# Optimization experiments

Measured on AMD Instinct MI355X. Metric: run time of the kernel, lower is better.

The kernel has to match this reference:

```python
import jax, jax.numpy as jnp
import numpy as np

D = 128  # input_depth == output_depth
NUM_NODES_PATTERN = np.tile(np.array([32, 48, 64, 96], dtype=np.int64), 64)  # G=256 graphs


def _build_indices(nn_np):
    """Per pair-entry (row-major within each n_g x n_g block): global row node,
    global col node, graph id, diagonal mask; plus per-node graph id / size."""
    G = len(nn_np)
    offs = np.zeros(G, dtype=np.int64)
    offs[1:] = np.cumsum(nn_np)[:-1]
    rows_l, cols_l, g_l, diag_l = [], [], [], []
    for gi, (n, o) in enumerate(zip(nn_np, offs)):
        i = np.repeat(np.arange(n, dtype=np.int64), n)  # row index within block
        j = np.tile(np.arange(n, dtype=np.int64), n)    # col index within block
        rows_l.append(o + i)
        cols_l.append(o + j)
        g_l.append(np.full(n * n, gi, dtype=np.int64))
        diag_l.append(i == j)
    rows = np.concatenate(rows_l)
    cols = np.concatenate(cols_l)
    g_edge = np.concatenate(g_l)
    diag = np.concatenate(diag_l)
    g_node = np.repeat(np.arange(G, dtype=np.int64), nn_np)  # graph of each node
    n_node = np.repeat(nn_np, nn_np)                          # n_g of each node
    N = int(nn_np.sum())
    return rows, cols, g_edge, diag, g_node, n_node, N, G


def setup_inputs() -> dict:
    key = jax.random.key(0)
    nn_np = NUM_NODES_PATTERN
    E = int(np.sum(nn_np ** 2))  # 1,064,960 pair entries
    N = int(nn_np.sum())         # 15,360 nodes
    k1, k2, k3 = jax.random.split(key, 3)
    x = jax.random.normal(k1, (E, D), dtype=jnp.float32)
    coeffs = jax.random.normal(k2, (D, D, 5), dtype=jnp.float32) * float(np.sqrt(2.0) / (D + D))
    bias = jnp.zeros((1, D), dtype=jnp.float32)
    edges_index = jax.random.randint(k3, (2, E), 0, N, dtype=jnp.int64)  # unused by the layer
    num_nodes = jnp.asarray(nn_np)
    return {"x": x, "coeffs": coeffs, "bias": bias,
            "edges_index": edges_index, "num_nodes": num_nodes}


def reference(x, coeffs, bias, edges_index, num_nodes):
    # edges_index is unused, matching the original forward.
    nn_np = np.asarray(num_nodes)
    rows, cols, g_edge, diag, g_node, n_node, N, G = _build_indices(nn_np)
    seg = jax.ops.segment_sum
    diag_m = jnp.asarray(diag)[:, None].astype(x.dtype)  # [E,1]
    n = jnp.asarray(n_node).astype(x.dtype)[:, None]     # [N,1] block size per node

    op1 = seg(x * diag_m, jnp.asarray(rows), num_segments=N)          # diag part (unnormalized)
    op3 = seg(x, jnp.asarray(rows), num_segments=N) / n               # row sums / n
    op4 = seg(x, jnp.asarray(cols), num_segments=N) / n               # col sums / n
    diag_g = seg(x * diag_m, jnp.asarray(g_edge), num_segments=G)     # [G,d] trace per graph
    all_g = seg(x, jnp.asarray(g_edge), num_segments=G)               # [G,d] total sum per graph
    gn = jnp.asarray(g_node)
    op2 = diag_g[gn] / n                                              # trace broadcast / n
    op5 = all_g[gn] / (n * n)                                         # total broadcast / n^2

    ops = jnp.stack([op1, op2, op3, op4, op5], axis=2)                # [N, d, 5]
    out = jnp.einsum('dsb,ndb->ns', coeffs, ops) + bias               # [N, output_depth]
    return out
```

## Files before the change

### kernel.cpp

```cpp
#include <hip/hip_runtime.h>

#define D 128


template<int CTRL>
__device__ __forceinline__ float f_dpp_add(float v) {
    return v + __int_as_float(__builtin_amdgcn_update_dpp(
        0, __float_as_int(v), CTRL, 0xF, 0xF, true));
}

#define DPP_ROR8 0x128

__device__ __forceinline__ float f_xor16_sum(float v) {
#if __has_builtin(__builtin_amdgcn_permlane16_swap)
    typedef int v2i __attribute__((ext_vector_type(2)));
    v2i r = __builtin_amdgcn_permlane16_swap(__float_as_int(v), __float_as_int(v),
                                             false, false);
    return __int_as_float(r[0]) + __int_as_float(r[1]);
#else
    return v + __shfl_xor(v, 16);
#endif
}

__device__ __forceinline__ float f_xor32_sum(float v) {
#if __has_builtin(__builtin_amdgcn_permlane32_swap)
    typedef int v2i __attribute__((ext_vector_type(2)));
    v2i r = __builtin_amdgcn_permlane32_swap(__float_as_int(v), __float_as_int(v),
                                             false, false);
    return __int_as_float(r[0]) + __int_as_float(r[1]);
#else
    return v + __shfl_xor(v, 32);
#endif
}

__device__ __forceinline__ void f4add(float4& a, const float4& b) {
    a.x += b.x; a.y += b.y; a.z += b.z; a.w += b.w;
}

__device__ __forceinline__ void f4_jreduce_full(float4& a) {
    a.x = f_dpp_add<DPP_ROR8>(a.x);
    a.y = f_dpp_add<DPP_ROR8>(a.y);
    a.z = f_dpp_add<DPP_ROR8>(a.z);
    a.w = f_dpp_add<DPP_ROR8>(a.w);
    a.x = f_xor16_sum(a.x);
    a.y = f_xor16_sum(a.y);
    a.z = f_xor16_sum(a.z);
    a.w = f_xor16_sum(a.w);
    a.x = f_xor32_sum(a.x);
    a.y = f_xor32_sum(a.y);
    a.z = f_xor32_sum(a.z);
    a.w = f_xor32_sum(a.w);
}

template<int N>
__device__ __forceinline__ void run_class(const float* __restrict__ x,
                                          long ebase, int o, int gidx, int chunk,
                                          float* __restrict__ diagG,
                                          float* __restrict__ rowG,
                                          float* __restrict__ colG,
                                          float* __restrict__ trG,
                                          float* __restrict__ totG,
                                          float4* __restrict__ rowtile ,
                                          float4* __restrict__ red     ) {
    constexpr int NW = (N < 64 ? N / 8 : 8);
    const int tid = threadIdx.x;
    const int l   = tid & 63;
    const int w   = tid >> 6;
    const int f4  = l & 7;
    const int j0  = tid >> 3;
    constexpr bool TWO = (N > 64);
    const bool act0 = (j0 < N);
    const bool act1 = TWO && (w < 4);
    const float invn = 1.0f / (float)N;

    const float4* x4 = reinterpret_cast<const float4*>(x);
    const long istride = (long)N * 32;
    const long e0 = (ebase + j0) * 32 + chunk * 8 + f4;

    float4 c0 = {0,0,0,0}, c1 = {0,0,0,0};

    int buf = 0;
    for (int t0 = 0; t0 < N; t0 += 16, buf ^= 1) {
        if (act0) {
            const float4* p0 = x4 + e0 + (long)t0 * istride;
            const float4* p1 = p0 + 64L * 32;
            float4* wt = rowtile + ((buf * 16) * 8 + w) * 8 + f4;
#pragma unroll 4
            for (int r = 0; r < 16; ++r) {
                float4 v = p0[(long)r * istride];
                f4add(c0, v);
                if (TWO && act1) {
                    float4 u = p1[(long)r * istride];
                    f4add(c1, u);
                    f4add(v, u);
                }
                f4_jreduce_full(v);
                if (l < 8) wt[r * 64] = v;
            }
        }
        __syncthreads();
        {
            const int rr = tid >> 5;
            const int dd = tid & 31;
            const float* rp = reinterpret_cast<const float*>(rowtile)
                            + (buf * 16 + rr) * 256 + dd;
            float acc = 0.f;
#pragma unroll
            for (int w2 = 0; w2 < NW; ++w2) acc += rp[w2 * 32];
            rowG[(long)(o + t0 + rr) * D + chunk * 32 + dd] = acc * invn;
        }
    }

    float4 d0 = {0,0,0,0}, d1 = {0,0,0,0};
    if (act0) d0 = x4[e0 + (long)j0 * istride];
    if (TWO && act1) d1 = x4[e0 + 64L * 32 + (long)(j0 + 64) * istride];

    float4* diag4 = reinterpret_cast<float4*>(diagG);
    float4* col4  = reinterpret_cast<float4*>(colG);
    if (act0) {
        diag4[(long)(o + j0) * 32 + chunk * 8 + f4] = d0;
        col4 [(long)(o + j0) * 32 + chunk * 8 + f4] = c0;
    }
    if (TWO && act1) {
        diag4[(long)(o + j0 + 64) * 32 + chunk * 8 + f4] = d1;
        col4 [(long)(o + j0 + 64) * 32 + chunk * 8 + f4] = c1;
    }

    {
        float4 td = d0; if (TWO) f4add(td, d1);
        float4 tc = c0; if (TWO) f4add(tc, c1);
        f4_jreduce_full(td);
        f4_jreduce_full(tc);
        if (l < 8) {
            red[w * 8 + f4]      = td;
            red[64 + w * 8 + f4] = tc;
        }
    }
    __syncthreads();
    float4* tr4  = reinterpret_cast<float4*>(trG);
    float4* tot4 = reinterpret_cast<float4*>(totG);
    if (tid < 8) {
        float4 a = {0,0,0,0};
#pragma unroll
        for (int w2 = 0; w2 < NW; ++w2) f4add(a, red[w2 * 8 + tid]);
        tr4[gidx * 32 + chunk * 8 + tid] = a;
    } else if (tid < 16) {
        const int f = tid - 8;
        float4 a = {0,0,0,0};
#pragma unroll
        for (int w2 = 0; w2 < NW; ++w2) f4add(a, red[64 + w2 * 8 + f]);
        tot4[gidx * 32 + chunk * 8 + f] = a;
    }
}

__global__ __launch_bounds__(512) void k1_reduce(const float* __restrict__ x,
                                                 float* __restrict__ diagG,
                                                 float* __restrict__ rowG,
                                                 float* __restrict__ colG,
                                                 float* __restrict__ trG,
                                                 float* __restrict__ totG) {
    __shared__ float4 rowtile[2048];
    __shared__ float4 red[128];

    const int b  = blockIdx.x;
    const int bb = b & 255;
    const int k  = bb >> 2;
    const int chunk = bb & 3;

    if (b < 256) {
        run_class<96>(x, 16640L * k + 7424, 240 * k + 144, 4 * k + 3, chunk, diagG, rowG, colG, trG, totG, rowtile, red);
    } else if (b < 512) {
        run_class<64>(x, 16640L * k + 3328, 240 * k + 80, 4 * k + 2, chunk, diagG, rowG, colG, trG, totG, rowtile, red);
    } else if (b < 768) {
        run_class<48>(x, 16640L * k + 1024, 240 * k + 32, 4 * k + 1, chunk, diagG, rowG, colG, trG, totG, rowtile, red);
    } else {
        run_class<32>(x, 16640L * k, 240 * k, 4 * k, chunk, diagG, rowG, colG, trG, totG, rowtile, red);
    }
}

__global__ void k0_transpose(const float* __restrict__ coeffs, float* __restrict__ Wt) {
    int d = blockIdx.x;
    int s = threadIdx.x;
    const float* cp = coeffs + ((long)d * D + s) * 5;
#pragma unroll
    for (int b = 0; b < 5; ++b) Wt[b * (D * D) + d * D + s] = cp[b];
}

__global__ __launch_bounds__(128) void k2_pg(const float* __restrict__ trG,
                                             const float* __restrict__ totG,
                                             const float* __restrict__ Wt,
                                             const float* __restrict__ bias,
                                             float* __restrict__ pg) {
    __shared__ float tr[D], tt[D];
    const int ns_[4] = {32, 48, 64, 96};
    int g = blockIdx.x;
    int c = g & 3;
    float invn = 1.0f / (float)ns_[c];

    int s = threadIdx.x;
    tr[s] = trG[g * D + s] * invn;
    tt[s] = totG[g * D + s] * invn * invn;
    __syncthreads();

    const float* W1 = Wt + 1 * D * D;
    const float* W4 = Wt + 4 * D * D;
    float acc = 0.f;
#pragma unroll 4
    for (int dd = 0; dd < D; ++dd)
        acc += W1[dd * D + s] * tr[dd] + W4[dd * D + s] * tt[dd];
    pg[g * D + s] = bias[s] + acc;
}

__global__ __launch_bounds__(512) void k3_gemm(const float* __restrict__ diagG,
                                               const float* __restrict__ rowG,
                                               const float* __restrict__ colG,
                                               const float* __restrict__ Wt,
                                               const float* __restrict__ pg,
                                               float* __restrict__ out) {
    __shared__ __align__(16) float ash[3][64][D];
    __shared__ int gish[64];
    const int nd0 = blockIdx.x * 64;
    const int tid = threadIdx.x;

    const float4* diag4 = reinterpret_cast<const float4*>(diagG);
    const float4* row4  = reinterpret_cast<const float4*>(rowG);
    const float4* col4  = reinterpret_cast<const float4*>(colG);

    for (int idx = tid; idx < 64 * 32; idx += 512) {
        int nn = idx >> 5;
        int q  = idx & 31;
        int nd = nd0 + nn;
        int p  = nd / 240;
        int r  = nd - p * 240;
        int c, n;
        if (r < 32)       { c = 0; n = 32; }
        else if (r < 80)  { c = 1; n = 48; }
        else if (r < 144) { c = 2; n = 64; }
        else              { c = 3; n = 96; }
        float invn = 1.0f / (float)n;
        float4 dv = diag4[(long)nd * 32 + q];
        float4 rv = row4[(long)nd * 32 + q];
        float4 cv = col4[(long)nd * 32 + q];
        cv.x *= invn; cv.y *= invn; cv.z *= invn; cv.w *= invn;
        *reinterpret_cast<float4*>(&ash[0][nn][q * 4]) = dv;
        *reinterpret_cast<float4*>(&ash[1][nn][q * 4]) = rv;
        *reinterpret_cast<float4*>(&ash[2][nn][q * 4]) = cv;
        if (q == 0) gish[nn] = 4 * p + c;
    }
    __syncthreads();

    const int s4 = tid & 31;
    const int nq = tid >> 5;
    const float* W0 = Wt;
    const float* W2 = Wt + 2 * D * D;
    const float* W3 = Wt + 3 * D * D;

    float4 acc[4];
#pragma unroll
    for (int a = 0; a < 4; ++a) acc[a] = make_float4(0.f, 0.f, 0.f, 0.f);

    for (int d4 = 0; d4 < 32; ++d4) {
        float4 w0[4], w2[4], w3[4];
#pragma unroll
        for (int dd = 0; dd < 4; ++dd) {
            const int d = d4 * 4 + dd;
            w0[dd] = *reinterpret_cast<const float4*>(&W0[d * D + s4 * 4]);
            w2[dd] = *reinterpret_cast<const float4*>(&W2[d * D + s4 * 4]);
            w3[dd] = *reinterpret_cast<const float4*>(&W3[d * D + s4 * 4]);
        }
#pragma unroll
        for (int a = 0; a < 4; ++a) {
            const int nn = nq * 4 + a;
            float4 a0 = *reinterpret_cast<const float4*>(&ash[0][nn][d4 * 4]);
            float4 a1 = *reinterpret_cast<const float4*>(&ash[1][nn][d4 * 4]);
            float4 a2 = *reinterpret_cast<const float4*>(&ash[2][nn][d4 * 4]);
            const float* a0f = reinterpret_cast<const float*>(&a0);
            const float* a1f = reinterpret_cast<const float*>(&a1);
            const float* a2f = reinterpret_cast<const float*>(&a2);
#pragma unroll
            for (int dd = 0; dd < 4; ++dd) {
                acc[a].x += w0[dd].x * a0f[dd] + w2[dd].x * a1f[dd] + w3[dd].x * a2f[dd];
                acc[a].y += w0[dd].y * a0f[dd] + w2[dd].y * a1f[dd] + w3[dd].y * a2f[dd];
                acc[a].z += w0[dd].z * a0f[dd] + w2[dd].z * a1f[dd] + w3[dd].z * a2f[dd];
                acc[a].w += w0[dd].w * a0f[dd] + w2[dd].w * a1f[dd] + w3[dd].w * a2f[dd];
            }
        }
    }

#pragma unroll
    for (int a = 0; a < 4; ++a) {
        const int nn = nq * 4 + a;
        const int nd = nd0 + nn;
        const int g  = gish[nn];
        float4 pgv = *reinterpret_cast<const float4*>(&pg[g * D + s4 * 4]);
        float4 r_;
        r_.x = acc[a].x + pgv.x;
        r_.y = acc[a].y + pgv.y;
        r_.z = acc[a].z + pgv.z;
        r_.w = acc[a].w + pgv.w;
        *reinterpret_cast<float4*>(&out[(long)nd * D + s4 * 4]) = r_;
    }
}

extern "C" void kernel_launch(void* const* d_in, const int* in_sizes, int n_in,
                              void* d_out, int out_size, void* d_ws, size_t ws_size,
                              hipStream_t stream) {
    const float* x      = (const float*)d_in[0];
    const float* coeffs = (const float*)d_in[1];
    const float* bias   = (const float*)d_in[2];

    float* ws    = (float*)d_ws;
    float* Wt    = ws;
    float* diagG = Wt + 81920;
    float* rowG  = diagG + 1966080;
    float* colG  = rowG + 1966080;
    float* pg    = colG + 1966080;
    float* trG   = pg + 32768;
    float* totG  = trG + 32768;
    float* out   = (float*)d_out;

    k0_transpose<<<128, 128, 0, stream>>>(coeffs, Wt);
    k1_reduce<<<1024, 512, 0, stream>>>(x, diagG, rowG, colG, trG, totG);
    k2_pg<<<256, 128, 0, stream>>>(trG, totG, Wt, bias, pg);
    k3_gemm<<<240, 512, 0, stream>>>(diagG, rowG, colG, Wt, pg, out);
}
```

Measured before the change: 202.7 us.

## Split reduction into per-class kernels over row blocks with atomic column/graph sums

Replaces the single reduction kernel, where each block walked a whole graph block for one feature chunk, with four templated kernels (one per graph size) whose blocks each handle only 16 rows. Column sums and per-graph trace and total sums are now built with float atomic adds into zeroed buffers, which needs an added memset. The goal is much more block-level parallelism and occupancy for streaming x, at the cost of many atomics, extra launches and a non-deterministic summation order.

```diff
diff --git a/kernel.cpp b/kernel.cpp
--- a/kernel.cpp
+++ b/kernel.cpp
@@ -52,129 +52,96 @@
     a.w = f_xor32_sum(a.w);
 }
 
-template<int N>
-__device__ __forceinline__ void run_class(const float* __restrict__ x,
-                                          long ebase, int o, int gidx, int chunk,
-                                          float* __restrict__ diagG,
-                                          float* __restrict__ rowG,
-                                          float* __restrict__ colG,
-                                          float* __restrict__ trG,
-                                          float* __restrict__ totG,
-                                          float4* __restrict__ rowtile ,
-                                          float4* __restrict__ red     ) {
-    constexpr int NW = (N < 64 ? N / 8 : 8);
+template<int N, int WPE>
+__global__ __launch_bounds__(N * 8, WPE)
+void k1_class(const float* __restrict__ x,
+              float* __restrict__ diagG, float* __restrict__ rowG,
+              float* __restrict__ colG, float* __restrict__ trG,
+              float* __restrict__ totG,
+              int EP, int NP, int CI) {
+    constexpr int NW  = N / 8;
+    constexpr int NRB = N / 16;
+    __shared__ __align__(16) float4 rowtile[16 * NW * 8];
+    __shared__ __align__(16) float4 red[2 * NW * 8];
+
     const int tid = threadIdx.x;
     const int l   = tid & 63;
     const int w   = tid >> 6;
     const int f4  = l & 7;
     const int j0  = tid >> 3;
-    constexpr bool TWO = (N > 64);
-    const bool act0 = (j0 < N);
-    const bool act1 = TWO && (w < 4);
+
+    const int b  = blockIdx.x;
+    const int rb = b % NRB;
+    const int ch = (b / NRB) & 3;
+    const int k  = b / (NRB * 4);
+    const long ebase = 16640L * k + EP;
+    const int  o     = 240 * k + NP;
+    const int  gi    = 4 * k + CI;
+    const int  r0    = rb * 16;
     const float invn = 1.0f / (float)N;
 
     const float4* x4 = reinterpret_cast<const float4*>(x);
     const long istride = (long)N * 32;
-    const long e0 = (ebase + j0) * 32 + chunk * 8 + f4;
-
-    float4 c0 = {0,0,0,0}, c1 = {0,0,0,0};
-
-    int buf = 0;
-    for (int t0 = 0; t0 < N; t0 += 16, buf ^= 1) {
-        if (act0) {
-            const float4* p0 = x4 + e0 + (long)t0 * istride;
-            const float4* p1 = p0 + 64L * 32;
-            float4* wt = rowtile + ((buf * 16) * 8 + w) * 8 + f4;
+    const long e0 = (ebase + (long)r0 * N + j0) * 32 + ch * 8 + f4;
+
+    float4 c0 = {0,0,0,0};
 #pragma unroll 4
-            for (int r = 0; r < 16; ++r) {
-                float4 v = p0[(long)r * istride];
-                f4add(c0, v);
-                if (TWO && act1) {
-                    float4 u = p1[(long)r * istride];
-                    f4add(c1, u);
-                    f4add(v, u);
-                }
-                f4_jreduce_full(v);
-                if (l < 8) wt[r * 64] = v;
-            }
-        }
-        __syncthreads();
-        {
-            const int rr = tid >> 5;
-            const int dd = tid & 31;
-            const float* rp = reinterpret_cast<const float*>(rowtile)
-                            + (buf * 16 + rr) * 256 + dd;
-            float acc = 0.f;
-#pragma unroll
-            for (int w2 = 0; w2 < NW; ++w2) acc += rp[w2 * 32];
-            rowG[(long)(o + t0 + rr) * D + chunk * 32 + dd] = acc * invn;
-        }
-    }
-
-    float4 d0 = {0,0,0,0}, d1 = {0,0,0,0};
-    if (act0) d0 = x4[e0 + (long)j0 * istride];
-    if (TWO && act1) d1 = x4[e0 + 64L * 32 + (long)(j0 + 64) * istride];
-
-    float4* diag4 = reinterpret_cast<float4*>(diagG);
-    float4* col4  = reinterpret_cast<float4*>(colG);
-    if (act0) {
-        diag4[(long)(o + j0) * 32 + chunk * 8 + f4] = d0;
-        col4 [(long)(o + j0) * 32 + chunk * 8 + f4] = c0;
-    }
-    if (TWO && act1) {
-        diag4[(long)(o + j0 + 64) * 32 + chunk * 8 + f4] = d1;
-        col4 [(long)(o + j0 + 64) * 32 + chunk * 8 + f4] = c1;
+    for (int r = 0; r < 16; ++r) {
+        float4 v = x4[e0 + (long)r * istride];
+        f4add(c0, v);
+        f4_jreduce_full(v);
+        if (l < 8) rowtile[(r * NW + w) * 8 + f4] = v;
+    }
+    __syncthreads();
+
+    for (int idx = tid; idx < 512; idx += N * 8) {
+        const int rr = idx >> 5;
+        const int dd = idx & 31;
+        const float* rp = reinterpret_cast<const float*>(rowtile) + rr * NW * 32 + dd;
+        float acc = 0.f;
+#pragma unroll
+        for (int w2 = 0; w2 < NW; ++w2) acc += rp[w2 * 32];
+        rowG[(long)(o + r0 + rr) * D + ch * 32 + dd] = acc * invn;
     }
 
     {
-        float4 td = d0; if (TWO) f4add(td, d1);
-        float4 tc = c0; if (TWO) f4add(tc, c1);
-        f4_jreduce_full(td);
-        f4_jreduce_full(tc);
-        if (l < 8) {
-            red[w * 8 + f4]      = td;
-            red[64 + w * 8 + f4] = tc;
-        }
+        float* cg = &colG[(long)(o + j0) * D + ch * 32 + f4 * 4];
+        unsafeAtomicAdd(cg + 0, c0.x);
+        unsafeAtomicAdd(cg + 1, c0.y);
+        unsafeAtomicAdd(cg + 2, c0.z);
+        unsafeAtomicAdd(cg + 3, c0.w);
+    }
+
+    float4 d0 = {0,0,0,0};
+    const bool hasdiag = (j0 >= r0) && (j0 < r0 + 16);
+    if (hasdiag) {
+        d0 = x4[(ebase + (long)j0 * N + j0) * 32 + ch * 8 + f4];
+        reinterpret_cast<float4*>(diagG)[(long)(o + j0) * 32 + ch * 8 + f4] = d0;
+    }
+
+    float4 td = d0, tc = c0;
+    f4_jreduce_full(td);
+    f4_jreduce_full(tc);
+    if (l < 8) {
+        red[w * 8 + f4]          = td;
+        red[NW * 8 + w * 8 + f4] = tc;
     }
     __syncthreads();
-    float4* tr4  = reinterpret_cast<float4*>(trG);
-    float4* tot4 = reinterpret_cast<float4*>(totG);
     if (tid < 8) {
         float4 a = {0,0,0,0};
 #pragma unroll
         for (int w2 = 0; w2 < NW; ++w2) f4add(a, red[w2 * 8 + tid]);
-        tr4[gidx * 32 + chunk * 8 + tid] = a;
+        float* tg = &trG[gi * D + ch * 32 + tid * 4];
+        unsafeAtomicAdd(tg + 0, a.x); unsafeAtomicAdd(tg + 1, a.y);
+        unsafeAtomicAdd(tg + 2, a.z); unsafeAtomicAdd(tg + 3, a.w);
     } else if (tid < 16) {
         const int f = tid - 8;
         float4 a = {0,0,0,0};
 #pragma unroll
-        for (int w2 = 0; w2 < NW; ++w2) f4add(a, red[64 + w2 * 8 + f]);
-        tot4[gidx * 32 + chunk * 8 + f] = a;
-    }
-}
-
-__global__ __launch_bounds__(512) void k1_reduce(const float* __restrict__ x,
-                                                 float* __restrict__ diagG,
-                                                 float* __restrict__ rowG,
-                                                 float* __restrict__ colG,
-                                                 float* __restrict__ trG,
-                                                 float* __restrict__ totG) {
-    __shared__ float4 rowtile[2048];
-    __shared__ float4 red[128];
-
-    const int b  = blockIdx.x;
-    const int bb = b & 255;
-    const int k  = bb >> 2;
-    const int chunk = bb & 3;
-
-    if (b < 256) {
-        run_class<96>(x, 16640L * k + 7424, 240 * k + 144, 4 * k + 3, chunk, diagG, rowG, colG, trG, totG, rowtile, red);
-    } else if (b < 512) {
-        run_class<64>(x, 16640L * k + 3328, 240 * k + 80, 4 * k + 2, chunk, diagG, rowG, colG, trG, totG, rowtile, red);
-    } else if (b < 768) {
-        run_class<48>(x, 16640L * k + 1024, 240 * k + 32, 4 * k + 1, chunk, diagG, rowG, colG, trG, totG, rowtile, red);
-    } else {
-        run_class<32>(x, 16640L * k, 240 * k, 4 * k, chunk, diagG, rowG, colG, trG, totG, rowtile, red);
+        for (int w2 = 0; w2 < NW; ++w2) f4add(a, red[NW * 8 + w2 * 8 + f]);
+        float* tg = &totG[gi * D + ch * 32 + f * 4];
+        unsafeAtomicAdd(tg + 0, a.x); unsafeAtomicAdd(tg + 1, a.y);
+        unsafeAtomicAdd(tg + 2, a.z); unsafeAtomicAdd(tg + 3, a.w);
     }
 }
 
@@ -314,13 +281,20 @@
     float* diagG = Wt + 81920;
     float* rowG  = diagG + 1966080;
     float* colG  = rowG + 1966080;
-    float* pg    = colG + 1966080;
-    float* trG   = pg + 32768;
+    float* trG   = colG + 1966080;
     float* totG  = trG + 32768;
+    float* pg    = totG + 32768;
     float* out   = (float*)d_out;
 
+    hipMemsetAsync(colG, 0, (1966080 + 32768 + 32768) * sizeof(float), stream);
+
     k0_transpose<<<128, 128, 0, stream>>>(coeffs, Wt);
-    k1_reduce<<<1024, 512, 0, stream>>>(x, diagG, rowG, colG, trG, totG);
+
+    k1_class<96, 6><<<1536, 768, 0, stream>>>(x, diagG, rowG, colG, trG, totG, 7424, 144, 3);
+    k1_class<64, 8><<<1024, 512, 0, stream>>>(x, diagG, rowG, colG, trG, totG, 3328,  80, 2);
+    k1_class<48, 8><<< 768, 384, 0, stream>>>(x, diagG, rowG, colG, trG, totG, 1024,  32, 1);
+    k1_class<32, 8><<< 512, 256, 0, stream>>>(x, diagG, rowG, colG, trG, totG,    0,   0, 0);
+
     k2_pg<<<256, 128, 0, stream>>>(trG, totG, Wt, bias, pg);
     k3_gemm<<<240, 512, 0, stream>>>(diagG, rowG, colG, Wt, pg, out);
 }
```

Result: slower. 266.2 us (+31.3%).

## Restructure block reduction: warps walk rows, keep column sums in registers

Applied to the files above, without the earlier changes.

The per-graph reduction kernel now assigns each wave whole rows of the pair block, with lanes covering columns in groups of 8. Row sums are reduced within the wave and column partials are held in registers (one float4 per column group). The old design had every thread own a column, staged row partials through a double-buffered shared tile and needed a barrier per 16 rows. The new code issues more independent loads per thread and removes the per-tile barriers. In exchange it merges column, trace and total partials through shared-memory atomics, and the N=96 case keeps 12 float4 accumulators, which raises register pressure.

```diff
diff --git a/kernel.cpp b/kernel.cpp
--- a/kernel.cpp
+++ b/kernel.cpp
@@ -60,96 +60,80 @@
                                           float* __restrict__ colG,
                                           float* __restrict__ trG,
                                           float* __restrict__ totG,
-                                          float4* __restrict__ rowtile ,
-                                          float4* __restrict__ red     ) {
-    constexpr int NW = (N < 64 ? N / 8 : 8);
-    const int tid = threadIdx.x;
-    const int l   = tid & 63;
-    const int w   = tid >> 6;
-    const int f4  = l & 7;
-    const int j0  = tid >> 3;
-    constexpr bool TWO = (N > 64);
-    const bool act0 = (j0 < N);
-    const bool act1 = TWO && (w < 4);
+                                          float* __restrict__ colshare ,
+                                          float* __restrict__ trshare  ,
+                                          float* __restrict__ totshare ) {
+    constexpr int CG = N / 8;
+    const int tid  = threadIdx.x;
+    const int l    = tid & 63;
+    const int w    = tid >> 6;
+    const int f4   = l & 7;
+    const int jsub = l >> 3;
     const float invn = 1.0f / (float)N;
 
-    const float4* x4 = reinterpret_cast<const float4*>(x);
-    const long istride = (long)N * 32;
-    const long e0 = (ebase + j0) * 32 + chunk * 8 + f4;
-
-    float4 c0 = {0,0,0,0}, c1 = {0,0,0,0};
-
-    int buf = 0;
-    for (int t0 = 0; t0 < N; t0 += 16, buf ^= 1) {
-        if (act0) {
-            const float4* p0 = x4 + e0 + (long)t0 * istride;
-            const float4* p1 = p0 + 64L * 32;
-            float4* wt = rowtile + ((buf * 16) * 8 + w) * 8 + f4;
-#pragma unroll 4
-            for (int r = 0; r < 16; ++r) {
-                float4 v = p0[(long)r * istride];
-                f4add(c0, v);
-                if (TWO && act1) {
-                    float4 u = p1[(long)r * istride];
-                    f4add(c1, u);
-                    f4add(v, u);
-                }
-                f4_jreduce_full(v);
-                if (l < 8) wt[r * 64] = v;
-            }
+    for (int idx = tid; idx < N * 33; idx += 512) colshare[idx] = 0.f;
+    if (tid < 32) { trshare[tid] = 0.f; totshare[tid] = 0.f; }
+    __syncthreads();
+
+    const float4* x4    = reinterpret_cast<const float4*>(x);
+    float4*       diag4 = reinterpret_cast<float4*>(diagG);
+    float4*       row4  = reinterpret_cast<float4*>(rowG);
+
+    float4 colacc[CG];
+#pragma unroll
+    for (int cg = 0; cg < CG; ++cg) colacc[cg] = make_float4(0.f, 0.f, 0.f, 0.f);
+    float4 tracc = make_float4(0.f, 0.f, 0.f, 0.f);
+
+    for (int t = 0; t < N / 8; ++t) {
+        const int i = w + 8 * t;
+        const float4* rp = x4 + (ebase + (long)i * N + jsub) * 32 + chunk * 8 + f4;
+        float4 racc = make_float4(0.f, 0.f, 0.f, 0.f);
+#pragma unroll
+        for (int cg = 0; cg < CG; ++cg) {
+            float4 v = rp[cg * 256];
+            f4add(racc, v);
+            f4add(colacc[cg], v);
         }
-        __syncthreads();
-        {
-            const int rr = tid >> 5;
-            const int dd = tid & 31;
-            const float* rp = reinterpret_cast<const float*>(rowtile)
-                            + (buf * 16 + rr) * 256 + dd;
-            float acc = 0.f;
-#pragma unroll
-            for (int w2 = 0; w2 < NW; ++w2) acc += rp[w2 * 32];
-            rowG[(long)(o + t0 + rr) * D + chunk * 32 + dd] = acc * invn;
+        f4_jreduce_full(racc);
+        if (l < 8) {
+            float4 dv = x4[(ebase + (long)i * N + i) * 32 + chunk * 8 + f4];
+            diag4[(long)(o + i) * 32 + chunk * 8 + f4] = dv;
+            f4add(tracc, dv);
+            float4 rv;
+            rv.x = racc.x * invn; rv.y = racc.y * invn;
+            rv.z = racc.z * invn; rv.w = racc.w * invn;
+            row4[(long)(o + i) * 32 + chunk * 8 + f4] = rv;
         }
     }
 
-    float4 d0 = {0,0,0,0}, d1 = {0,0,0,0};
-    if (act0) d0 = x4[e0 + (long)j0 * istride];
-    if (TWO && act1) d1 = x4[e0 + 64L * 32 + (long)(j0 + 64) * istride];
-
-    float4* diag4 = reinterpret_cast<float4*>(diagG);
-    float4* col4  = reinterpret_cast<float4*>(colG);
-    if (act0) {
-        diag4[(long)(o + j0) * 32 + chunk * 8 + f4] = d0;
-        col4 [(long)(o + j0) * 32 + chunk * 8 + f4] = c0;
-    }
-    if (TWO && act1) {
-        diag4[(long)(o + j0 + 64) * 32 + chunk * 8 + f4] = d1;
-        col4 [(long)(o + j0 + 64) * 32 + chunk * 8 + f4] = c1;
-    }
-
-    {
-        float4 td = d0; if (TWO) f4add(td, d1);
-        float4 tc = c0; if (TWO) f4add(tc, c1);
-        f4_jreduce_full(td);
-        f4_jreduce_full(tc);
-        if (l < 8) {
-            red[w * 8 + f4]      = td;
-            red[64 + w * 8 + f4] = tc;
-        }
-    }
-    __syncthreads();
-    float4* tr4  = reinterpret_cast<float4*>(trG);
-    float4* tot4 = reinterpret_cast<float4*>(totG);
-    if (tid < 8) {
-        float4 a = {0,0,0,0};
-#pragma unroll
-        for (int w2 = 0; w2 < NW; ++w2) f4add(a, red[w2 * 8 + tid]);
-        tr4[gidx * 32 + chunk * 8 + tid] = a;
-    } else if (tid < 16) {
-        const int f = tid - 8;
-        float4 a = {0,0,0,0};
-#pragma unroll
-        for (int w2 = 0; w2 < NW; ++w2) f4add(a, red[64 + w2 * 8 + f]);
-        tot4[gidx * 32 + chunk * 8 + f] = a;
+#pragma unroll
+    for (int cg = 0; cg < CG; ++cg) {
+        float* cs = &colshare[(8 * cg + jsub) * 33 + f4 * 4];
+        atomicAdd(cs + 0, colacc[cg].x);
+        atomicAdd(cs + 1, colacc[cg].y);
+        atomicAdd(cs + 2, colacc[cg].z);
+        atomicAdd(cs + 3, colacc[cg].w);
+    }
+    if (l < 8) {
+        float* ts = &trshare[f4 * 4];
+        atomicAdd(ts + 0, tracc.x); atomicAdd(ts + 1, tracc.y);
+        atomicAdd(ts + 2, tracc.z); atomicAdd(ts + 3, tracc.w);
+    }
+    __syncthreads();
+
+    float tot = 0.f;
+    for (int idx = tid; idx < N * 32; idx += 512) {
+        const int col = idx >> 5;
+        const int dd  = idx & 31;
+        const float cv = colshare[col * 33 + dd];
+        colG[(long)(o + col) * D + chunk * 32 + dd] = cv;
+        tot += cv;
+    }
+    atomicAdd(&totshare[tid & 31], tot);
+    __syncthreads();
+    if (tid < 32) {
+        trG [gidx * D + chunk * 32 + tid] = trshare[tid];
+        totG[gidx * D + chunk * 32 + tid] = totshare[tid];
     }
 }
 
@@ -159,8 +143,9 @@
                                                  float* __restrict__ colG,
                                                  float* __restrict__ trG,
                                                  float* __restrict__ totG) {
-    __shared__ float4 rowtile[2048];
-    __shared__ float4 red[128];
+    __shared__ float colshare[96 * 33];
+    __shared__ float trshare[32];
+    __shared__ float totshare[32];
 
     const int b  = blockIdx.x;
     const int bb = b & 255;
@@ -168,13 +153,13 @@
     const int chunk = bb & 3;
 
     if (b < 256) {
-        run_class<96>(x, 16640L * k + 7424, 240 * k + 144, 4 * k + 3, chunk, diagG, rowG, colG, trG, totG, rowtile, red);
+        run_class<96>(x, 16640L * k + 7424, 240 * k + 144, 4 * k + 3, chunk, diagG, rowG, colG, trG, totG, colshare, trshare, totshare);
     } else if (b < 512) {
-        run_class<64>(x, 16640L * k + 3328, 240 * k + 80, 4 * k + 2, chunk, diagG, rowG, colG, trG, totG, rowtile, red);
+        run_class<64>(x, 16640L * k + 3328, 240 * k + 80, 4 * k + 2, chunk, diagG, rowG, colG, trG, totG, colshare, trshare, totshare);
     } else if (b < 768) {
-        run_class<48>(x, 16640L * k + 1024, 240 * k + 32, 4 * k + 1, chunk, diagG, rowG, colG, trG, totG, rowtile, red);
+        run_class<48>(x, 16640L * k + 1024, 240 * k + 32, 4 * k + 1, chunk, diagG, rowG, colG, trG, totG, colshare, trshare, totshare);
     } else {
-        run_class<32>(x, 16640L * k, 240 * k, 4 * k, chunk, diagG, rowG, colG, trG, totG, rowtile, red);
+        run_class<32>(x, 16640L * k, 240 * k, 4 * k, chunk, diagG, rowG, colG, trG, totG, colshare, trshare, totshare);
     }
 }
 
```

Result: slower. 246.4 us (+21.6%).
